# Performance work log

Hardware: AMD Instinct MI355X
Metric: run time of the kernel (lower is better)

Reference implementation:

```python
import jax, jax.numpy as jnp
import numpy as np

MEAN = np.array([0.485, 0.456, 0.406], np.float32).reshape(1, 3, 1, 1)
STD = np.array([0.229, 0.224, 0.225], np.float32).reshape(1, 3, 1, 1)
BN_EPS = 1e-5


def _srm_kernels():
    """Standard SRM 30-filter 5x5 high-pass bank (Fridrich) -> [30,1,5,5]."""
    ks = []
    Z = lambda: np.zeros((5, 5), np.float32)
    D8 = [(-1, 0), (-1, 1), (0, 1), (1, 1), (1, 0), (1, -1), (0, -1), (-1, -1)]
    for dy, dx in D8:  # 8 first-order
        k = Z(); k[2, 2] = -1.0; k[2 + dy, 2 + dx] = 1.0; ks.append(k)
    for dy, dx in D8[:4]:  # 4 second-order
        k = Z(); k[2, 2] = -2.0; k[2 + dy, 2 + dx] = 1.0; k[2 - dy, 2 - dx] = 1.0
        ks.append(k / 2.0)
    for dy, dx in D8:  # 8 third-order
        k = Z()
        k[2 - dy, 2 - dx] = -1.0; k[2, 2] = 3.0
        k[2 + dy, 2 + dx] = -3.0; k[2 + 2 * dy, 2 + 2 * dx] = 1.0
        ks.append(k / 3.0)
    sq3 = np.array([[-1, 2, -1], [2, -4, 2], [-1, 2, -1]], np.float32) / 4.0
    k = Z(); k[1:4, 1:4] = sq3; ks.append(k)  # SQUARE 3x3
    sq5 = np.array([[-1, 2, -2, 2, -1], [2, -6, 8, -6, 2], [-2, 8, -12, 8, -2],
                    [2, -6, 8, -6, 2], [-1, 2, -2, 2, -1]], np.float32) / 12.0
    ks.append(sq5)  # SQUARE 5x5
    e3 = np.array([[-1, 2, -1], [2, -4, 2], [0, 0, 0]], np.float32) / 4.0
    for r in range(4):  # 4 EDGE 3x3
        k = Z(); k[1:4, 1:4] = np.rot90(e3, r); ks.append(k)
    e5 = np.array([[-1, 2, -2, 2, -1], [2, -6, 8, -6, 2], [-2, 8, -12, 8, -2],
                   [0, 0, 0, 0, 0], [0, 0, 0, 0, 0]], np.float32) / 4.0
    for r in range(4):  # 4 EDGE 5x5
        ks.append(np.rot90(e5, r).copy())
    return np.stack(ks)[:, None]  # [30,1,5,5]

SRM_K = jnp.asarray(_srm_kernels())
GAUSS_K = jnp.asarray((np.outer([1, 4, 6, 4, 1], [1, 4, 6, 4, 1]) / 256.0)
                      .astype(np.float32))[None, None]  # [1,1,5,5]
CFA_K = jnp.asarray((np.array([[0, 1, 0], [1, 0, 1], [0, 1, 0]], np.float32) / 4.0))[None, None]


def conv2d(x, w, b=None):
    y = jax.lax.conv_general_dilated(x, w, (1, 1), 'SAME',
                                     dimension_numbers=('NCHW', 'OIHW', 'NCHW'))
    if b is not None:
        y = y + b[None, :, None, None]
    return y


def batchnorm(x, g, b, m, v):
    inv = jax.lax.rsqrt(v + BN_EPS)
    return (x - m[None, :, None, None]) * (g * inv)[None, :, None, None] + b[None, :, None, None]


def extract_features(x):
    """Batched PRNU(1) + SRM(30) + CFA(1) feature maps -> [B,32,H,W]."""
    img = jnp.clip(x * STD + MEAN, 0.0, 1.0)  # denormalize
    gray = (0.299 * img[:, 0] + 0.587 * img[:, 1] + 0.114 * img[:, 2])[:, None]  # [B,1,H,W]
    prnu = gray - conv2d(gray, GAUSS_K)            # denoise-subtract noise residual
    srm = conv2d(gray, SRM_K)                       # [B,30,H,W]
    green = img[:, 1:2]
    cfa = green - conv2d(green, CFA_K)              # CFA interpolation residual
    return jnp.concatenate([prnu, srm, cfa], axis=1)  # [B,32,H,W]


def setup_inputs() -> dict:
    key = jax.random.key(0)
    ks = jax.random.split(key, 16)
    B, H, W = 16, 256, 256
    d = {"x": jax.random.normal(ks[0], (B, 3, H, W), jnp.float32)}
    cins = [32, 64, 64, 64]
    for i in range(4):
        cin, co = cins[i], 64
        scale = (2.0 / (cin * 9)) ** 0.5  # kaiming
        d[f"w{i+1}"] = jax.random.normal(ks[1 + i], (co, cin, 3, 3), jnp.float32) * scale
        d[f"b{i+1}"] = jnp.zeros((co,), jnp.float32)
        d[f"g{i+1}"] = jnp.ones((co,), jnp.float32)
        d[f"be{i+1}"] = jnp.zeros((co,), jnp.float32)
        d[f"m{i+1}"] = jax.random.normal(ks[5 + i], (co,), jnp.float32) * 0.1
        d[f"v{i+1}"] = jax.random.uniform(ks[9 + i], (co,), jnp.float32, 0.5, 1.5)
    return d


def reference(x, w1, b1, g1, be1, m1, v1, w2, b2, g2, be2, m2, v2,
              w3, b3, g3, be3, m3, v3, w4, b4, g4, be4, m4, v4):
    h = extract_features(x)
    for w, b, g, be, m, v in ((w1, b1, g1, be1, m1, v1), (w2, b2, g2, be2, m2, v2),
                              (w3, b3, g3, be3, m3, v3), (w4, b4, g4, be4, m4, v4)):
        h = jax.nn.relu(batchnorm(conv2d(h, w, b), g, be, m, v))
    return h  # [B,64,H,W]
```

## Files before the change

### kernel.cpp

```cpp
#include <hip/hip_runtime.h>
#include <hip/hip_bf16.h>
#include <cstddef>

#define B_ 16
#define H_ 256
#define W_ 256
#define HW_ (H_ * W_)
#define P_ 258


typedef _Float16 half8 __attribute__((ext_vector_type(8)));
typedef float floatx4 __attribute__((ext_vector_type(4)));

__device__ __forceinline__ void gload_lds16(void* lds, const void* g) {
  __builtin_amdgcn_global_load_lds(
      (const __attribute__((address_space(1))) unsigned int*)g,
      (__attribute__((address_space(3))) unsigned int*)lds, 16, 0, 0);
}

template <int NCG>
__global__ __launch_bounds__(256) void zero_border(_Float16* __restrict__ buf) {
  int idx = blockIdx.x * 256 + threadIdx.x;
  int total = 16 * NCG * 1028;
  if (idx >= total) return;
  int p = idx % 1028;
  int rest = idx / 1028;
  int cg = rest % NCG;
  int b = rest / NCG;
  int row, col;
  if (p < 258) { row = 0; col = p; }
  else if (p < 516) { row = 257; col = p - 258; }
  else if (p < 772) { row = p - 515; col = 0; }
  else { row = p - 771; col = 257; }
  *(floatx4*)&buf[(((size_t)(b * NCG + cg) * P_ + row) * P_ + col) * 8] =
      (floatx4)0.f;
}

__global__ __launch_bounds__(256) void feat_kernel(const float* __restrict__ x,
                                                   _Float16* __restrict__ F) {
  __shared__ float sg[36][37];
  __shared__ float sgr[36][37];

  const int b = blockIdx.z;
  const int y0 = blockIdx.y * 32;
  const int x0 = blockIdx.x * 32;
  const float* xb = x + (size_t)b * 3 * HW_;

  for (int i = threadIdx.x; i < 36 * 36; i += 256) {
    int iy = i / 36, ix = i % 36;
    int gy = y0 + iy - 2, gx = x0 + ix - 2;
    float gray = 0.f, green = 0.f;
    if (gy >= 0 && gy < H_ && gx >= 0 && gx < W_) {
      int idx = gy * W_ + gx;
      float r = fminf(fmaxf(xb[idx] * 0.229f + 0.485f, 0.f), 1.f);
      float g = fminf(fmaxf(xb[idx + HW_] * 0.224f + 0.456f, 0.f), 1.f);
      float bl = fminf(fmaxf(xb[idx + 2 * HW_] * 0.225f + 0.406f, 0.f), 1.f);
      gray = 0.299f * r + 0.587f * g + 0.114f * bl;
      green = g;
    }
    sg[iy][ix] = gray;
    sgr[iy][ix] = green;
  }
  __syncthreads();

  for (int p = threadIdx.x; p < 32 * 32; p += 256) {
    const int py = p >> 5, px = p & 31;
    const int ly = py + 2, lx = px + 2;
#define G(dy, dx) sg[ly + (dy)][lx + (dx)]
    float f[32];
    const float c = G(0, 0);

    {
      const float ga[5] = {1.f, 4.f, 6.f, 4.f, 1.f};
      float s = 0.f;
#pragma unroll
      for (int i = 0; i < 5; i++) {
        float rs = 0.f;
#pragma unroll
        for (int j = 0; j < 5; j++) rs += ga[j] * G(i - 2, j - 2);
        s += ga[i] * rs;
      }
      f[0] = c - s * (1.0f / 256.0f);
    }

    const int dy8[8] = {-1, -1, 0, 1, 1, 1, 0, -1};
    const int dx8[8] = {0, 1, 1, 1, 0, -1, -1, -1};

#pragma unroll
    for (int k = 0; k < 8; k++) f[1 + k] = G(dy8[k], dx8[k]) - c;
#pragma unroll
    for (int k = 0; k < 4; k++)
      f[9 + k] = 0.5f * (G(dy8[k], dx8[k]) + G(-dy8[k], -dx8[k])) - c;
#pragma unroll
    for (int k = 0; k < 8; k++)
      f[13 + k] = (-G(-dy8[k], -dx8[k]) + 3.f * c - 3.f * G(dy8[k], dx8[k]) +
                   G(2 * dy8[k], 2 * dx8[k])) * (1.f / 3.f);

    {
      const float sq3[3][3] = {{-1, 2, -1}, {2, -4, 2}, {-1, 2, -1}};
      float s = 0.f;
#pragma unroll
      for (int i = 0; i < 3; i++)
#pragma unroll
        for (int j = 0; j < 3; j++) s += sq3[i][j] * G(i - 1, j - 1);
      f[21] = s * 0.25f;
    }
    {
      const float sq5[5][5] = {{-1, 2, -2, 2, -1},
                               {2, -6, 8, -6, 2},
                               {-2, 8, -12, 8, -2},
                               {2, -6, 8, -6, 2},
                               {-1, 2, -2, 2, -1}};
      float s = 0.f;
#pragma unroll
      for (int i = 0; i < 5; i++)
#pragma unroll
        for (int j = 0; j < 5; j++) s += sq5[i][j] * G(i - 2, j - 2);
      f[22] = s * (1.0f / 12.0f);
    }
    {
      const float e3[3][3] = {{-1, 2, -1}, {2, -4, 2}, {0, 0, 0}};
      float s0 = 0.f, s1 = 0.f, s2 = 0.f, s3 = 0.f;
#pragma unroll
      for (int i = 0; i < 3; i++)
#pragma unroll
        for (int j = 0; j < 3; j++) {
          float v = G(i - 1, j - 1);
          s0 += e3[i][j] * v;
          s1 += e3[j][2 - i] * v;
          s2 += e3[2 - i][2 - j] * v;
          s3 += e3[2 - j][i] * v;
        }
      f[23] = s0 * 0.25f;
      f[24] = s1 * 0.25f;
      f[25] = s2 * 0.25f;
      f[26] = s3 * 0.25f;
    }
    {
      const float e5[5][5] = {{-1, 2, -2, 2, -1},
                              {2, -6, 8, -6, 2},
                              {-2, 8, -12, 8, -2},
                              {0, 0, 0, 0, 0},
                              {0, 0, 0, 0, 0}};
      float s0 = 0.f, s1 = 0.f, s2 = 0.f, s3 = 0.f;
#pragma unroll
      for (int i = 0; i < 5; i++)
#pragma unroll
        for (int j = 0; j < 5; j++) {
          float v = G(i - 2, j - 2);
          s0 += e5[i][j] * v;
          s1 += e5[j][4 - i] * v;
          s2 += e5[4 - i][4 - j] * v;
          s3 += e5[4 - j][i] * v;
        }
      f[27] = s0 * 0.25f;
      f[28] = s1 * 0.25f;
      f[29] = s2 * 0.25f;
      f[30] = s3 * 0.25f;
    }
    {
      float gc = sgr[ly][lx];
      f[31] = gc - 0.25f * (sgr[ly - 1][lx] + sgr[ly][lx - 1] +
                            sgr[ly][lx + 1] + sgr[ly + 1][lx]);
    }
#undef G

    _Float16 h[32];
#pragma unroll
    for (int cc = 0; cc < 32; cc++) h[cc] = (_Float16)f[cc];
    const floatx4* src = (const floatx4*)h;
#pragma unroll
    for (int cg = 0; cg < 4; cg++)
      *(floatx4*)&F[(((size_t)(b * 4 + cg) * P_ + (y0 + py + 1)) * P_ +
                     (x0 + px + 1)) * 8] = src[cg];
  }
}

__global__ void wprep_kernel(const float* __restrict__ w,
                             const float* __restrict__ bias,
                             const float* __restrict__ g,
                             const float* __restrict__ be,
                             const float* __restrict__ m,
                             const float* __restrict__ v,
                             _Float16* __restrict__ wp,
                             float* __restrict__ sc, float* __restrict__ sh,
                             int cin) {
  int i = blockIdx.x * 256 + threadIdx.x;
  int total = cin * 9 * 64;
  if (i < total) {
    int j = i & 7;
    int co = (i >> 3) & 63;
    int rest = i >> 9;
    int t = rest % 9;
    int qc = rest / 9;
    int ci = qc * 8 + j;
    wp[i] = (_Float16)w[((size_t)co * cin + ci) * 9 + t];
  }
  if (i < 64) {
    float s = g[i] * rsqrtf(v[i] + 1e-5f);
    sc[i] = s;
    sh[i] = be[i] + (bias[i] - m[i]) * s;
  }
}

template <int CIN, bool FINAL>
__global__ __launch_bounds__(256, 2) void conv_mfma(
    const _Float16* __restrict__ in, const _Float16* __restrict__ wp,
    const float* __restrict__ sc, const float* __restrict__ sh,
    void* __restrict__ outv) {
  __shared__ char smem[42240 + 36864];
  _Float16(*s_in)[10][66][8] = (_Float16(*)[10][66][8])smem;
  _Float16(*s_w)[9][64][8] = (_Float16(*)[9][64][8])(smem + 42240);

  const int tid = threadIdx.x;
  const int b = blockIdx.z;
  const int y0 = blockIdx.y * 8;
  const int x0 = blockIdx.x * 64;
  const int wid = tid >> 6;
  const int lane = tid & 63;
  const int quad = lane >> 4;
  const int ln = lane & 15;

  floatx4 acc[8][4];
#pragma unroll
  for (int mt = 0; mt < 8; mt++)
#pragma unroll
    for (int nt = 0; nt < 4; nt++) acc[mt][nt] = (floatx4)0.f;

  for (int kc = 0; kc < CIN / 32; kc++) {
    __syncthreads();
    for (int i = tid; i < 2640; i += 256) {
      int q = i / 660, rem = i % 660;
      int row = rem / 66, col = rem % 66;
      gload_lds16(smem + i * 16,
                  &in[(((size_t)(b * (CIN / 8) + kc * 4 + q) * P_ +
                        (y0 + row)) * P_ + (x0 + col)) * 8]);
    }
    for (int i = tid; i < 2304; i += 256) {
      gload_lds16(smem + 42240 + i * 16, wp + ((size_t)kc * 2304 + i) * 8);
    }
    __syncthreads();

#pragma unroll
    for (int t = 0; t < 9; t++) {
      const int ty = t / 3, tx = t % 3;
      half8 a[8], bb[4];
#pragma unroll
      for (int nt = 0; nt < 4; nt++)
        bb[nt] = *(const half8*)&s_w[quad][t][nt * 16 + ln][0];
#pragma unroll
      for (int mt = 0; mt < 8; mt++)
        a[mt] = *(const half8*)
            &s_in[quad][2 * wid + ty + (mt >> 2)][(mt & 3) * 16 + ln + tx][0];
#pragma unroll
      for (int mt = 0; mt < 8; mt++)
#pragma unroll
        for (int nt = 0; nt < 4; nt++)
          acc[mt][nt] = __builtin_amdgcn_mfma_f32_16x16x32_f16(
              a[mt], bb[nt], acc[mt][nt], 0, 0, 0);
    }
  }

  if (FINAL) {
    float* out = (float*)outv;
#pragma unroll
    for (int nt = 0; nt < 4; nt++) {
      int co = nt * 16 + ln;
      float s = sc[co], t0 = sh[co];
#pragma unroll
      for (int mt = 0; mt < 8; mt++) {
        int y = y0 + 2 * wid + (mt >> 2);
        int xb = x0 + (mt & 3) * 16 + quad * 4;
        floatx4 vv;
#pragma unroll
        for (int r = 0; r < 4; r++) vv[r] = fmaxf(acc[mt][nt][r] * s + t0, 0.f);
        *(floatx4*)&out[(((size_t)b * 64 + co) * H_ + y) * W_ + xb] = vv;
      }
    }
  } else {
    __syncthreads();
    _Float16* s_out = (_Float16*)smem + wid * 8192;
#pragma unroll
    for (int nt = 0; nt < 4; nt++) {
      int co = nt * 16 + ln;
      float s = sc[co], t0 = sh[co];
      int cog = co >> 3, clo = co & 7;
#pragma unroll
      for (int mt = 0; mt < 8; mt++) {
        int pix0 = (mt >> 2) * 64 + (mt & 3) * 16 + quad * 4;
#pragma unroll
        for (int r = 0; r < 4; r++) {
          int pix = pix0 + r;
          s_out[pix * 64 + (((cog ^ (pix & 7)) << 3) | clo)] =
              (_Float16)fmaxf(acc[mt][nt][r] * s + t0, 0.f);
        }
      }
    }
    _Float16* out = (_Float16*)outv;
#pragma unroll
    for (int k = 0; k < 16; k++) {
      int rw = k >> 3, cog = k & 7;
      int pix = rw * 64 + lane;
      int gy = y0 + 2 * wid + rw + 1, gx = x0 + lane + 1;
      *(floatx4*)&out[(((size_t)(b * 8 + cog) * P_ + gy) * P_ + gx) * 8] =
          *(const floatx4*)&s_out[pix * 64 + ((cog ^ (lane & 7)) << 3)];
    }
  }
}

extern "C" void kernel_launch(void* const* d_in, const int* in_sizes, int n_in,
                              void* d_out, int out_size, void* d_ws,
                              size_t ws_size, hipStream_t stream) {
  const float* x = (const float*)d_in[0];
#define LAYER_PTRS(i)                                                       \
  const float* w##i = (const float*)d_in[1 + ((i)-1) * 6 + 0];              \
  const float* b##i = (const float*)d_in[1 + ((i)-1) * 6 + 1];              \
  const float* g##i = (const float*)d_in[1 + ((i)-1) * 6 + 2];              \
  const float* be##i = (const float*)d_in[1 + ((i)-1) * 6 + 3];             \
  const float* m##i = (const float*)d_in[1 + ((i)-1) * 6 + 4];              \
  const float* v##i = (const float*)d_in[1 + ((i)-1) * 6 + 5];
  LAYER_PTRS(1)
  LAYER_PTRS(2)
  LAYER_PTRS(3)
  LAYER_PTRS(4)
#undef LAYER_PTRS

  char* ws = (char*)d_ws;
  const size_t featB = (size_t)16 * 4 * P_ * P_ * 8 * 2;
  const size_t actB64 = (size_t)16 * 8 * P_ * P_ * 8 * 2;
  _Float16* feat = (_Float16*)ws;
  _Float16* actA = (_Float16*)(ws + featB);
  _Float16* actB = (_Float16*)(ws + featB + actB64);
  char* wbase = ws + featB + 2 * actB64;
  _Float16* wp1 = (_Float16*)(wbase);
  _Float16* wp2 = (_Float16*)(wbase + 36864);
  _Float16* wp3 = (_Float16*)(wbase + 36864 + 73728);
  _Float16* wp4 = (_Float16*)(wbase + 36864 + 2 * 73728);
  float* scsh = (float*)(wbase + 36864 + 3 * 73728);
  float *sc1 = scsh, *sh1 = scsh + 64;
  float *sc2 = scsh + 128, *sh2 = scsh + 192;
  float *sc3 = scsh + 256, *sh3 = scsh + 320;
  float *sc4 = scsh + 384, *sh4 = scsh + 448;

  wprep_kernel<<<72, 256, 0, stream>>>(w1, b1, g1, be1, m1, v1, wp1, sc1, sh1, 32);
  wprep_kernel<<<144, 256, 0, stream>>>(w2, b2, g2, be2, m2, v2, wp2, sc2, sh2, 64);
  wprep_kernel<<<144, 256, 0, stream>>>(w3, b3, g3, be3, m3, v3, wp3, sc3, sh3, 64);
  wprep_kernel<<<144, 256, 0, stream>>>(w4, b4, g4, be4, m4, v4, wp4, sc4, sh4, 64);

  zero_border<4><<<257, 256, 0, stream>>>(feat);
  zero_border<8><<<514, 256, 0, stream>>>(actA);
  zero_border<8><<<514, 256, 0, stream>>>(actB);

  dim3 fgrid(W_ / 32, H_ / 32, B_);
  feat_kernel<<<fgrid, 256, 0, stream>>>(x, feat);

  dim3 cgrid(W_ / 64, H_ / 8, B_);
  conv_mfma<32, false><<<cgrid, 256, 0, stream>>>(feat, wp1, sc1, sh1, actA);
  conv_mfma<64, false><<<cgrid, 256, 0, stream>>>(actA, wp2, sc2, sh2, actB);
  conv_mfma<64, false><<<cgrid, 256, 0, stream>>>(actB, wp3, sc3, sh3, actA);
  conv_mfma<64, true><<<cgrid, 256, 0, stream>>>(actA, wp4, sc4, sh4, d_out);
}
```

Before: 643.7 us.

## Stage full-CIN input and weights in LDS once; merge prep launches

For the 64-channel conv layers, the whole input tile and all weights are now loaded into LDS up front. This replaces the previous two chunked load/sync rounds, removing one barrier and serialized load phase per block. The cost is LDS use that roughly doubles to about 158KB, with launch bounds dropping to 1 block per CU, so latency hiding now depends on a single block. Separately, the four weight-prep launches and the three border-zeroing launches are merged into one launch each, and an explicit waitcnt is added before the output store.

Measured after the change: 739.7 us. +14.9%, slower.

```diff
diff --git a/kernel.cpp b/kernel.cpp
--- a/kernel.cpp
+++ b/kernel.cpp
@@ -18,21 +18,27 @@
       (__attribute__((address_space(3))) unsigned int*)lds, 16, 0, 0);
 }
 
-template <int NCG>
-__global__ __launch_bounds__(256) void zero_border(_Float16* __restrict__ buf) {
+__global__ __launch_bounds__(256) void zero_border3(_Float16* __restrict__ f,
+                                                    _Float16* __restrict__ a,
+                                                    _Float16* __restrict__ bb) {
   int idx = blockIdx.x * 256 + threadIdx.x;
-  int total = 16 * NCG * 1028;
+  int total = 16 * 20 * 1028;
   if (idx >= total) return;
   int p = idx % 1028;
   int rest = idx / 1028;
-  int cg = rest % NCG;
-  int b = rest / NCG;
+  int cg = rest % 20;
+  int b = rest / 20;
+  _Float16* buf;
+  int ncg, c;
+  if (cg < 4) { buf = f; ncg = 4; c = cg; }
+  else if (cg < 12) { buf = a; ncg = 8; c = cg - 4; }
+  else { buf = bb; ncg = 8; c = cg - 12; }
   int row, col;
   if (p < 258) { row = 0; col = p; }
   else if (p < 516) { row = 257; col = p - 258; }
   else if (p < 772) { row = p - 515; col = 0; }
   else { row = p - 771; col = 257; }
-  *(floatx4*)&buf[(((size_t)(b * NCG + cg) * P_ + row) * P_ + col) * 8] =
+  *(floatx4*)&buf[(((size_t)(b * ncg + c) * P_ + row) * P_ + col) * 8] =
       (floatx4)0.f;
 }
 
@@ -176,15 +182,32 @@
   }
 }
 
-__global__ void wprep_kernel(const float* __restrict__ w,
-                             const float* __restrict__ bias,
-                             const float* __restrict__ g,
-                             const float* __restrict__ be,
-                             const float* __restrict__ m,
-                             const float* __restrict__ v,
-                             _Float16* __restrict__ wp,
-                             float* __restrict__ sc, float* __restrict__ sh,
-                             int cin) {
+__global__ void wprep4_kernel(
+    const float* __restrict__ w1, const float* __restrict__ b1,
+    const float* __restrict__ g1, const float* __restrict__ be1,
+    const float* __restrict__ m1, const float* __restrict__ v1,
+    const float* __restrict__ w2, const float* __restrict__ b2,
+    const float* __restrict__ g2, const float* __restrict__ be2,
+    const float* __restrict__ m2, const float* __restrict__ v2,
+    const float* __restrict__ w3, const float* __restrict__ b3,
+    const float* __restrict__ g3, const float* __restrict__ be3,
+    const float* __restrict__ m3, const float* __restrict__ v3,
+    const float* __restrict__ w4, const float* __restrict__ b4,
+    const float* __restrict__ g4, const float* __restrict__ be4,
+    const float* __restrict__ m4, const float* __restrict__ v4,
+    _Float16* __restrict__ wp1, _Float16* __restrict__ wp2,
+    _Float16* __restrict__ wp3, _Float16* __restrict__ wp4,
+    float* __restrict__ scsh) {
+  const int layer = blockIdx.y;
+  const float *w, *bias, *g, *be, *m, *v;
+  _Float16* wp;
+  int cin;
+  switch (layer) {
+    case 0: w = w1; bias = b1; g = g1; be = be1; m = m1; v = v1; wp = wp1; cin = 32; break;
+    case 1: w = w2; bias = b2; g = g2; be = be2; m = m2; v = v2; wp = wp2; cin = 64; break;
+    case 2: w = w3; bias = b3; g = g3; be = be3; m = m3; v = v3; wp = wp3; cin = 64; break;
+    default: w = w4; bias = b4; g = g4; be = be4; m = m4; v = v4; wp = wp4; cin = 64; break;
+  }
   int i = blockIdx.x * 256 + threadIdx.x;
   int total = cin * 9 * 64;
   if (i < total) {
@@ -198,19 +221,25 @@
   }
   if (i < 64) {
     float s = g[i] * rsqrtf(v[i] + 1e-5f);
-    sc[i] = s;
-    sh[i] = be[i] + (bias[i] - m[i]) * s;
+    scsh[layer * 128 + i] = s;
+    scsh[layer * 128 + 64 + i] = be[i] + (bias[i] - m[i]) * s;
   }
 }
 
 template <int CIN, bool FINAL>
-__global__ __launch_bounds__(256, 2) void conv_mfma(
+__global__ __launch_bounds__(256, CIN == 32 ? 2 : 1) void conv_mfma(
     const _Float16* __restrict__ in, const _Float16* __restrict__ wp,
     const float* __restrict__ sc, const float* __restrict__ sh,
     void* __restrict__ outv) {
-  __shared__ char smem[42240 + 36864];
+  constexpr int NP = CIN / 8;
+  constexpr int IN_BYTES = NP * 10 * 66 * 8 * 2;
+  constexpr int W_BYTES = NP * 9 * 64 * 8 * 2;
+  constexpr int IN_UNITS = NP * 10 * 66;
+  constexpr int W_UNITS = W_BYTES / 16;
+
+  __shared__ char smem[IN_BYTES + W_BYTES];
   _Float16(*s_in)[10][66][8] = (_Float16(*)[10][66][8])smem;
-  _Float16(*s_w)[9][64][8] = (_Float16(*)[9][64][8])(smem + 42240);
+  _Float16(*s_w)[9][64][8] = (_Float16(*)[9][64][8])(smem + IN_BYTES);
 
   const int tid = threadIdx.x;
   const int b = blockIdx.z;
@@ -227,31 +256,31 @@
 #pragma unroll
     for (int nt = 0; nt < 4; nt++) acc[mt][nt] = (floatx4)0.f;
 
-  for (int kc = 0; kc < CIN / 32; kc++) {
-    __syncthreads();
-    for (int i = tid; i < 2640; i += 256) {
-      int q = i / 660, rem = i % 660;
-      int row = rem / 66, col = rem % 66;
-      gload_lds16(smem + i * 16,
-                  &in[(((size_t)(b * (CIN / 8) + kc * 4 + q) * P_ +
-                        (y0 + row)) * P_ + (x0 + col)) * 8]);
-    }
-    for (int i = tid; i < 2304; i += 256) {
-      gload_lds16(smem + 42240 + i * 16, wp + ((size_t)kc * 2304 + i) * 8);
-    }
-    __syncthreads();
-
+  for (int i = tid; i < IN_UNITS; i += 256) {
+    int q = i / 660, rem = i % 660;
+    int row = rem / 66, col = rem % 66;
+    gload_lds16(smem + i * 16,
+                &in[(((size_t)(b * NP + q) * P_ + (y0 + row)) * P_ +
+                     (x0 + col)) * 8]);
+  }
+  for (int i = tid; i < W_UNITS; i += 256) {
+    gload_lds16(smem + IN_BYTES + i * 16, wp + (size_t)i * 8);
+  }
+  __syncthreads();
+
+  for (int kc = 0; kc < NP / 4; kc++) {
 #pragma unroll
     for (int t = 0; t < 9; t++) {
       const int ty = t / 3, tx = t % 3;
       half8 a[8], bb[4];
 #pragma unroll
       for (int nt = 0; nt < 4; nt++)
-        bb[nt] = *(const half8*)&s_w[quad][t][nt * 16 + ln][0];
+        bb[nt] = *(const half8*)&s_w[kc * 4 + quad][t][nt * 16 + ln][0];
 #pragma unroll
       for (int mt = 0; mt < 8; mt++)
-        a[mt] = *(const half8*)
-            &s_in[quad][2 * wid + ty + (mt >> 2)][(mt & 3) * 16 + ln + tx][0];
+        a[mt] = *(const half8*)&s_in[kc * 4 + quad]
+                                    [2 * wid + ty + (mt >> 2)]
+                                    [(mt & 3) * 16 + ln + tx][0];
 #pragma unroll
       for (int mt = 0; mt < 8; mt++)
 #pragma unroll
@@ -296,6 +325,7 @@
         }
       }
     }
+    __builtin_amdgcn_s_waitcnt(0);
     _Float16* out = (_Float16*)outv;
 #pragma unroll
     for (int k = 0; k < 16; k++) {
@@ -342,14 +372,13 @@
   float *sc3 = scsh + 256, *sh3 = scsh + 320;
   float *sc4 = scsh + 384, *sh4 = scsh + 448;
 
-  wprep_kernel<<<72, 256, 0, stream>>>(w1, b1, g1, be1, m1, v1, wp1, sc1, sh1, 32);
-  wprep_kernel<<<144, 256, 0, stream>>>(w2, b2, g2, be2, m2, v2, wp2, sc2, sh2, 64);
-  wprep_kernel<<<144, 256, 0, stream>>>(w3, b3, g3, be3, m3, v3, wp3, sc3, sh3, 64);
-  wprep_kernel<<<144, 256, 0, stream>>>(w4, b4, g4, be4, m4, v4, wp4, sc4, sh4, 64);
-
-  zero_border<4><<<257, 256, 0, stream>>>(feat);
-  zero_border<8><<<514, 256, 0, stream>>>(actA);
-  zero_border<8><<<514, 256, 0, stream>>>(actB);
+  dim3 wgrid(144, 4);
+  wprep4_kernel<<<wgrid, 256, 0, stream>>>(
+      w1, b1, g1, be1, m1, v1, w2, b2, g2, be2, m2, v2,
+      w3, b3, g3, be3, m3, v3, w4, b4, g4, be4, m4, v4,
+      wp1, wp2, wp3, wp4, scsh);
+
+  zero_border3<<<1285, 256, 0, stream>>>(feat, actA, actB);
 
   dim3 fgrid(W_ / 32, H_ / 32, B_);
   feat_kernel<<<fgrid, 256, 0, stream>>>(x, feat);
```
